# Optimization experiments

Measured on AMD Instinct MI355X. Metric: run time of the kernel, lower is better.

## Reference

```python
import jax, jax.numpy as jnp
import numpy as np

B, L, D, H, DFF, V, NL = 8, 512, 1024, 16, 4096, 32000, 6
DH = D // H
EPS = 1e-5


def _layer_norm(x):
    # fresh nn.LayerNorm(d_model) each call: gamma=1, beta=0
    mu = jnp.mean(x, axis=-1, keepdims=True)
    var = jnp.var(x, axis=-1, keepdims=True)
    return (x - mu) / jnp.sqrt(var + EPS)


def _positional_encoding(seq_len, d_model, dtype):
    position = jnp.arange(seq_len, dtype=jnp.float32)[:, None]
    div_term = 1.0 / jnp.power(10000.0, jnp.arange(0, d_model, 2, dtype=jnp.float32) / d_model)
    pe = jnp.zeros((seq_len, d_model), dtype=jnp.float32)
    pe = pe.at[:, 0::2].set(jnp.sin(position * div_term))
    pe = pe.at[:, 1::2].set(jnp.cos(position * div_term))
    return pe.astype(dtype)  # [L, D]


def setup_inputs() -> dict:
    key = jax.random.key(0)
    ks = jax.random.split(key, 16)
    s = 0.02
    inp = {
        "sequence": jax.random.randint(ks[0], (B, L), 0, V),
        "segment_label": jax.random.randint(ks[1], (B, L), 0, 3),
        "tok_emb": jax.random.normal(ks[2], (V, D), jnp.float32) * s,
        "seg_emb": jax.random.normal(ks[3], (3, D), jnp.float32) * s,
        "Wq": jax.random.normal(ks[4], (NL, D, D), jnp.float32) * s,
        "bq": jnp.zeros((NL, D), jnp.float32),
        "Wk": jax.random.normal(ks[5], (NL, D, D), jnp.float32) * s,
        "bk": jnp.zeros((NL, D), jnp.float32),
        "Wv": jax.random.normal(ks[6], (NL, D, D), jnp.float32) * s,
        "bv": jnp.zeros((NL, D), jnp.float32),
        "Wo": jax.random.normal(ks[7], (NL, D, D), jnp.float32) * s,
        "bo": jnp.zeros((NL, D), jnp.float32),
        "W1": jax.random.normal(ks[8], (NL, D, DFF), jnp.float32) * s,
        "b1": jnp.zeros((NL, DFF), jnp.float32),
        "W2": jax.random.normal(ks[9], (NL, DFF, D), jnp.float32) * s,
        "b2": jnp.zeros((NL, D), jnp.float32),
    }
    return inp


def reference(sequence, segment_label, tok_emb, seg_emb, Wq, bq, Wk, bk, Wv, bv, Wo, bo, W1, b1, W2, b2):
    n_layers = Wq.shape[0]
    batch, seq_len = sequence.shape
    d_model = tok_emb.shape[1]
    n_heads = H
    dh = d_model // n_heads

    # pad mask: True where key token == 0; broadcast over heads and query positions
    pad = (sequence == 0)  # [B, Lk]
    mask = pad[:, None, None, :]  # [B, 1, 1, Lk]

    pe = _positional_encoding(seq_len, d_model, tok_emb.dtype)
    x = tok_emb[sequence] + pe[None, :, :] + seg_emb[segment_label]  # [B, L, D]

    for i in range(n_layers):
        residual = x
        # NOTE: original code uses a raw reshape [B, L, H*dh] -> [B, H, L, dh]
        # (no transpose); we replicate that exact math.
        q = (x @ Wq[i] + bq[i]).reshape(batch, n_heads, seq_len, dh)
        k = (x @ Wk[i] + bk[i]).reshape(batch, n_heads, seq_len, dh)
        v = (x @ Wv[i] + bv[i]).reshape(batch, n_heads, seq_len, dh)
        scores = jnp.einsum("bhqd,bhkd->bhqk", q, k) / jnp.sqrt(jnp.asarray(dh, x.dtype))
        scores = jnp.where(mask, jnp.asarray(-1e9, x.dtype), scores)
        attn = jax.nn.softmax(scores, axis=-1)
        context = jnp.einsum("bhqk,bhkd->bhqd", attn, v).reshape(batch, seq_len, n_heads * dh)
        out = context @ Wo[i] + bo[i]
        x = _layer_norm(out + residual)

        residual = x
        h = jax.nn.gelu(x @ W1[i] + b1[i], approximate=False)
        out = h @ W2[i] + b2[i]
        x = _layer_norm(residual + out)

    return x
```

## Files before the change

### kernel.cpp

```cpp
#include <hip/hip_runtime.h>
#include <cstdint>
#include <cstddef>

typedef unsigned short u16;
typedef __attribute__((ext_vector_type(8))) short short8;
typedef __attribute__((ext_vector_type(4))) float f32x4;

#define DEV __device__ __forceinline__

DEV float bf2f(u16 u) {
    union { float f; uint32_t i; } c; c.i = ((uint32_t)u) << 16; return c.f;
}
DEV u16 f2bf(float f) {
    union { float f; uint32_t i; } c; c.f = f;
    uint32_t r = c.i + 0x7FFF + ((c.i >> 16) & 1);
    return (u16)(r >> 16);
}

DEV void gload16(const void* g, void* l) {
    __builtin_amdgcn_global_load_lds(
        (const __attribute__((address_space(1))) void*)g,
        (__attribute__((address_space(3))) void*)l, 16, 0, 0);
}

template<int N> DEV void waitv() {
    if constexpr (N == 0)      asm volatile("s_waitcnt vmcnt(0)" ::: "memory");
    else if constexpr (N == 4) asm volatile("s_waitcnt vmcnt(4)" ::: "memory");
    else if constexpr (N == 8) asm volatile("s_waitcnt vmcnt(8)" ::: "memory");
    else                       asm volatile("s_waitcnt vmcnt(0)" ::: "memory");
}

template<int EPI>
__global__ __launch_bounds__(512)
void gemm_k64(const u16* __restrict__ Ablk, const u16* __restrict__ Bblk,
              void* __restrict__ C, const float* __restrict__ bias,
              const float* __restrict__ resid, int K, int Mtot, int Ntot)
{
    constexpr int THREADS = 512;
    constexpr int BM = 128, BN = 128;
    constexpr int MR = 4, NR = 2;
    __shared__ __align__(16) u16 As[3 * BM * 64];
    __shared__ __align__(16) u16 Bs[3 * BN * 64];

    const int tid = threadIdx.x, lane = tid & 63, wid = tid >> 6;
    const int wr = wid >> 2, wc = wid & 3;
    const int lr = lane & 15, lk = lane >> 4;
    const int m0 = blockIdx.x * BM, n0 = blockIdx.y * BN;
    const long planeA = (long)Mtot * 64, planeB = (long)Ntot * 64;

    f32x4 acc[MR][NR] = {};

    auto stageA = [&](int buf, int k0) {
#pragma unroll
        for (int i = 0; i < 2; ++i) {
            int ch = i * THREADS + tid;
            int row = ch >> 3, s = ch & 7, d = s ^ (row & 7);
            const u16* g = Ablk + (long)(k0 >> 6) * planeA + (long)(m0 + row) * 64 + d * 8;
            gload16(g, (char*)As + (size_t)buf * (BM * 128) + ch * 16);
        }
    };
    auto stageB = [&](int buf, int k0) {
#pragma unroll
        for (int i = 0; i < 2; ++i) {
            int ch = i * THREADS + tid;
            int row = ch >> 3, s = ch & 7, d = s ^ (row & 7);
            const u16* g = Bblk + (long)(k0 >> 6) * planeB + (long)(n0 + row) * 64 + d * 8;
            gload16(g, (char*)Bs + (size_t)buf * (BN * 128) + ch * 16);
        }
    };
    auto lds_off = [&](int row, int ks) -> int {
        return row * 64 + ((ks ^ (row & 7)) << 3);
    };

    const int nt = K >> 6;

    stageA(0, 0); stageB(0, 0);
    if (nt > 1) { stageA(1, 64); stageB(1, 64); }
    if (nt > 2) { stageA(2, 128); stageB(2, 128); }
    if (nt > 2)      waitv<8>();
    else if (nt > 1) waitv<4>();
    else             waitv<0>();
    __builtin_amdgcn_s_barrier();

    for (int k = 0; k < nt; ++k) {
        const int cur = k % 3;
        const u16* Ac = As + (size_t)cur * (BM * 64);
        const u16* Bc = Bs + (size_t)cur * (BN * 64);
        short8 af[2][MR], bf[2][NR];
#pragma unroll
        for (int h = 0; h < 2; ++h) {
#pragma unroll
            for (int m = 0; m < MR; ++m)
                af[h][m] = *(const short8*)(Ac + lds_off(wr * 64 + m * 16 + lr, h * 4 + lk));
#pragma unroll
            for (int n = 0; n < NR; ++n)
                bf[h][n] = *(const short8*)(Bc + lds_off(wc * 32 + n * 16 + lr, h * 4 + lk));
        }

        asm volatile("s_waitcnt lgkmcnt(0)" ::: "memory");
        __builtin_amdgcn_s_barrier();

        if (k + 3 < nt) { stageA(cur, (k + 3) * 64); stageB(cur, (k + 3) * 64); }

        __builtin_amdgcn_s_setprio(1);
#pragma unroll
        for (int h = 0; h < 2; ++h)
#pragma unroll
            for (int m = 0; m < MR; ++m)
#pragma unroll
                for (int n = 0; n < NR; ++n)
                    acc[m][n] = __builtin_amdgcn_mfma_f32_16x16x32_bf16(af[h][m], bf[h][n], acc[m][n], 0, 0, 0);
        __builtin_amdgcn_s_setprio(0);

        if (k + 1 < nt) {
            if (k + 4 <= nt)      waitv<8>();
            else if (k + 3 == nt) waitv<4>();
            else                  waitv<0>();
            __builtin_amdgcn_s_barrier();
        }
    }

#pragma unroll
    for (int m = 0; m < MR; ++m) {
        const int rowb = m0 + wr * 64 + m * 16 + (lane >> 4) * 4;
#pragma unroll
        for (int n = 0; n < NR; ++n) {
            const int col = n0 + wc * 32 + n * 16 + lr;
            const float bv = bias[col];
#pragma unroll
            for (int j = 0; j < 4; ++j) {
                float v = acc[m][n][j];
                if (EPI == 1) {
                    const long idx = (long)(rowb + j) * 1024 + col;
                    ((float*)C)[idx] = v + bv + resid[idx];
                } else if (EPI == 5) {
                    const long qidx = (long)(col >> 10) * 4194304L
                                    + (long)(rowb + j) * 1024 + (col & 1023);
                    ((u16*)C)[qidx] = f2bf(v + bv);
                } else {
                    float t = v + bv;
                    ((u16*)C)[(long)(col >> 6) * 262144L + (long)(rowb + j) * 64 + (col & 63)]
                        = f2bf(0.5f * t * (1.0f + erff(t * 0.70710678118654752f)));
                }
            }
        }
    }
}

__global__ __launch_bounds__(512)
void attn_kernel(const u16* __restrict__ Qb, const u16* __restrict__ Kb,
                 const u16* __restrict__ vt, const int* __restrict__ seq,
                 u16* __restrict__ ctxB)
{
    __shared__ __align__(16) u16 Ss[64 * 512];
    const int tid = threadIdx.x, lane = tid & 63, wid = tid >> 6;
    const int bh = blockIdx.y;
    const int b  = bh >> 4;
    const int q0 = blockIdx.x << 6;
    const u16* Qh = Qb + ((long)bh << 15) + (long)q0 * 64;
    const u16* Kh = Kb + ((long)bh << 15);
    const u16* Vh = vt + ((long)bh << 15);
    const int lr = lane & 15, lk = lane >> 4;

    f32x4 sacc[4][4] = {};
    {
        short8 af[4], bf[4];
#pragma unroll
        for (int s = 0; s < 2; ++s) {
#pragma unroll
            for (int m = 0; m < 4; ++m)
                af[m] = *(const short8*)(Qh + (long)(m * 16 + lr) * 64 + s * 32 + lk * 8);
#pragma unroll
            for (int n = 0; n < 4; ++n)
                bf[n] = *(const short8*)(Kh + (long)(wid * 64 + n * 16 + lr) * 64 + s * 32 + lk * 8);
#pragma unroll
            for (int m = 0; m < 4; ++m)
#pragma unroll
                for (int n = 0; n < 4; ++n)
                    sacc[m][n] = __builtin_amdgcn_mfma_f32_16x16x32_bf16(af[m], bf[n], sacc[m][n], 0, 0, 0);
        }
    }
#pragma unroll
    for (int m = 0; m < 4; ++m) {
#pragma unroll
        for (int n = 0; n < 4; ++n) {
            const int k = wid * 64 + n * 16 + lr;
#pragma unroll
            for (int j = 0; j < 4; ++j) {
                const int q = m * 16 + (lane >> 4) * 4 + j;
                const int col = (((k >> 3) ^ (q & 7)) << 3) | (k & 7);
                Ss[q * 512 + col] = f2bf(sacc[m][n][j] * 0.125f);
            }
        }
    }
    __syncthreads();

    const int* sq = seq + (b << 9) + (lane << 3);
    int msk[8];
#pragma unroll
    for (int i = 0; i < 8; ++i) msk[i] = sq[i];
#pragma unroll
    for (int r = 0; r < 8; ++r) {
        const int q = wid * 8 + r;
        u16* p = Ss + q * 512 + ((lane ^ (q & 7)) << 3);
        short8 raw = *(short8*)p;
        float v[8];
#pragma unroll
        for (int i = 0; i < 8; ++i)
            v[i] = (msk[i] == 0) ? -1e9f : bf2f((u16)raw[i]);
        float mx = v[0];
#pragma unroll
        for (int i = 1; i < 8; ++i) mx = fmaxf(mx, v[i]);
#pragma unroll
        for (int o = 32; o; o >>= 1) mx = fmaxf(mx, __shfl_xor(mx, o));
        float e[8], sum = 0.f;
#pragma unroll
        for (int i = 0; i < 8; ++i) { e[i] = expf(v[i] - mx); sum += e[i]; }
#pragma unroll
        for (int o = 32; o; o >>= 1) sum += __shfl_xor(sum, o);
        float rr = 1.0f / sum;
        short8 o8;
#pragma unroll
        for (int i = 0; i < 8; ++i) o8[i] = (short)f2bf(e[i] * rr);
        *(short8*)p = o8;
    }
    __syncthreads();

    const int wr = wid >> 1, wc2 = wid & 1;
    f32x4 pacc[2] = {};
#pragma unroll
    for (int ks = 0; ks < 16; ++ks) {
        const int qrow = wr * 16 + lr;
        short8 pa = *(const short8*)(Ss + qrow * 512 + (((ks * 4 + lk) ^ (qrow & 7)) << 3));
        short8 vb[2];
#pragma unroll
        for (int n = 0; n < 2; ++n) {
            const int d = wc2 * 32 + n * 16 + lr;
            vb[n] = *(const short8*)(Vh + (long)d * 512 + ks * 32 + lk * 8);
        }
#pragma unroll
        for (int n = 0; n < 2; ++n)
            pacc[n] = __builtin_amdgcn_mfma_f32_16x16x32_bf16(pa, vb[n], pacc[n], 0, 0, 0);
    }
#pragma unroll
    for (int n = 0; n < 2; ++n) {
        const int d = wc2 * 32 + n * 16 + lr;
#pragma unroll
        for (int j = 0; j < 4; ++j) {
            const int q = wr * 16 + (lane >> 4) * 4 + j;
            const long F = ((long)bh << 15) + (long)(q0 + q) * 64 + d;
            const long r = F >> 10;
            const int  c = (int)(F & 1023);
            ctxB[(long)(c >> 6) * 262144L + r * 64 + (c & 63)] = f2bf(pacc[n][j]);
        }
    }
}

__global__ __launch_bounds__(256)
void wconv_blk(const float* __restrict__ src, u16* __restrict__ dst,
               int N, int planeN, int row_off, long src_z, long dst_z)
{
    __shared__ __align__(16) float t[64][65];
    const int z = blockIdx.z;
    const int k0 = blockIdx.x * 64, n0 = blockIdx.y * 64;
    const float* s = src + (long)z * src_z + (long)k0 * N + n0;
    const int tid = threadIdx.x;
#pragma unroll
    for (int i = 0; i < 4; ++i) {
        int ch = (i << 8) + tid;
        int r = ch >> 4, c4 = ch & 15;
        float4 v = *(const float4*)(s + (long)r * N + c4 * 4);
        t[r][c4 * 4 + 0] = v.x; t[r][c4 * 4 + 1] = v.y;
        t[r][c4 * 4 + 2] = v.z; t[r][c4 * 4 + 3] = v.w;
    }
    __syncthreads();
    u16* d = dst + (long)z * dst_z + (long)blockIdx.x * planeN * 64 + (long)(row_off + n0) * 64;
#pragma unroll
    for (int i = 0; i < 4; ++i) {
        int ch = (i << 8) + tid;
        int c = ch >> 4, k4 = ch & 15;
        ushort4 o;
        o.x = f2bf(t[k4 * 4 + 0][c]);
        o.y = f2bf(t[k4 * 4 + 1][c]);
        o.z = f2bf(t[k4 * 4 + 2][c]);
        o.w = f2bf(t[k4 * 4 + 3][c]);
        *(ushort4*)(d + (long)c * 64 + k4 * 4) = o;
    }
}

__global__ __launch_bounds__(256)
void bconcat_kernel(const float* __restrict__ bq, const float* __restrict__ bk,
                    const float* __restrict__ bv, float* __restrict__ out)
{
    int i = blockIdx.x * 256 + threadIdx.x;
    int l = i / 3072, n = i % 3072;
    float v = (n < 1024) ? bq[l * 1024 + n]
            : (n < 2048) ? bk[l * 1024 + n - 1024]
                         : bv[l * 1024 + n - 2048];
    out[i] = v;
}

__global__ __launch_bounds__(256)
void embed_kernel(const int* __restrict__ seq, const int* __restrict__ seg,
                  const float* __restrict__ tok, const float* __restrict__ sege,
                  float* __restrict__ x, u16* __restrict__ xbB)
{
    long i = ((long)blockIdx.x << 8) + threadIdx.x;
    int d2 = (int)(i & 511);
    long bl = i >> 9;
    int l = (int)(bl & 511);
    int t = seq[bl];
    int g = seg[bl];
    float div = powf(10000.f, -(float)(2 * d2) * (1.0f / 1024.f));
    float arg = (float)l * div;
    float sv = sinf(arg), cv = cosf(arg);
    long toff = (long)t * 1024 + 2 * d2;
    long goff = (long)g * 1024 + 2 * d2;
    float x0 = tok[toff]     + sv + sege[goff];
    float x1 = tok[toff + 1] + cv + sege[goff + 1];
    long xo = (bl << 10) + 2 * d2;
    x[xo] = x0; x[xo + 1] = x1;
    const int c = 2 * d2;
    u16* p = xbB + (long)(c >> 6) * 262144L + bl * 64 + (c & 63);
    p[0] = f2bf(x0); p[1] = f2bf(x1);
}

__global__ __launch_bounds__(256)
void vtrans_kernel(const u16* __restrict__ Vb, u16* __restrict__ vt)
{
    __shared__ __align__(16) u16 t[64][72];
    const int bh = blockIdx.y;
    const int l0 = blockIdx.x << 6;
    const u16* src = Vb + ((long)bh << 15) + (long)l0 * 64;
    const int tid = threadIdx.x;
#pragma unroll
    for (int i = 0; i < 2; ++i) {
        int ch = (i << 8) + tid;
        int r = ch >> 3, c8 = ch & 7;
        short8 v = *(const short8*)(src + (long)r * 64 + (c8 << 3));
#pragma unroll
        for (int j = 0; j < 8; ++j) t[r][(c8 << 3) + j] = (u16)v[j];
    }
    __syncthreads();
    u16* d = vt + ((long)bh << 15) + l0;
#pragma unroll
    for (int i = 0; i < 2; ++i) {
        int ch = (i << 8) + tid;
        int dd = ch >> 3, l8 = ch & 7;
        short8 o;
#pragma unroll
        for (int j = 0; j < 8; ++j) o[j] = (short)t[(l8 << 3) + j][dd];
        *(short8*)(d + (long)dd * 512 + (l8 << 3)) = o;
    }
}

__global__ __launch_bounds__(256)
void ln_kernel(const float* __restrict__ in, float* __restrict__ xout, u16* __restrict__ xbB)
{
    const int row = blockIdx.x;
    const int tid = threadIdx.x;
    const float4 v = ((const float4*)(in + (long)row * 1024))[tid];
    float s = v.x + v.y + v.z + v.w;
#pragma unroll
    for (int o = 32; o; o >>= 1) s += __shfl_down(s, o);
    __shared__ float red[8];
    const int wid = tid >> 6, lane = tid & 63;
    if (lane == 0) red[wid] = s;
    __syncthreads();
    const float mean = (red[0] + red[1] + red[2] + red[3]) * (1.0f / 1024.f);
    const float dx = v.x - mean, dy = v.y - mean, dz = v.z - mean, dw = v.w - mean;
    float q = dx * dx + dy * dy + dz * dz + dw * dw;
#pragma unroll
    for (int o = 32; o; o >>= 1) q += __shfl_down(q, o);
    if (lane == 0) red[4 + wid] = q;
    __syncthreads();
    const float var = (red[4] + red[5] + red[6] + red[7]) * (1.0f / 1024.f);
    const float inv = rsqrtf(var + 1e-5f);
    float4 o4;
    o4.x = dx * inv; o4.y = dy * inv; o4.z = dz * inv; o4.w = dw * inv;
    ((float4*)(xout + (long)row * 1024))[tid] = o4;
    ushort4 ob;
    ob.x = f2bf(o4.x); ob.y = f2bf(o4.y); ob.z = f2bf(o4.z); ob.w = f2bf(o4.w);
    *(ushort4*)(xbB + (long)(tid >> 4) * 262144L + (long)row * 64 + (tid & 15) * 4) = ob;
}

extern "C" void kernel_launch(void* const* d_in, const int* in_sizes, int n_in,
                              void* d_out, int out_size, void* d_ws, size_t ws_size,
                              hipStream_t stream)
{
    const int*   seqp = (const int*)d_in[0];
    const int*   segp = (const int*)d_in[1];
    const float* tok  = (const float*)d_in[2];
    const float* sege = (const float*)d_in[3];
    const float* Wq = (const float*)d_in[4];  const float* bq = (const float*)d_in[5];
    const float* Wk = (const float*)d_in[6];  const float* bk = (const float*)d_in[7];
    const float* Wv = (const float*)d_in[8];  const float* bv = (const float*)d_in[9];
    const float* Wo = (const float*)d_in[10]; const float* bo = (const float*)d_in[11];
    const float* W1 = (const float*)d_in[12]; const float* b1 = (const float*)d_in[13];
    const float* W2 = (const float*)d_in[14]; const float* b2 = (const float*)d_in[15];

    char* w = (char*)d_ws;
    auto take = [&](size_t bytes) -> void* {
        void* p = (void*)w; w += (bytes + 255) & ~(size_t)255; return p;
    };
    float* x    = (float*)take(4096UL * 1024 * 4);
    u16*   xbB  = (u16*)  take(4096UL * 1024 * 2);
    float* tmp  = (float*)take(4096UL * 1024 * 4);
    u16*   hbuf = (u16*)  take(4096UL * 4096 * 2);
    u16*   qkv3 = (u16*)  take(3UL * 4096 * 1024 * 2);
    u16*   ctxB = (u16*)  take(4096UL * 1024 * 2);
    u16*   vt   = (u16*)  take(128UL * 64 * 512 * 2);
    u16*   qkvwB= (u16*)  take(6UL * 3072 * 1024 * 2);
    u16*   woB  = (u16*)  take(6UL * 1024 * 1024 * 2);
    u16*   w1B  = (u16*)  take(6UL * 4096 * 1024 * 2);
    u16*   w2B  = (u16*)  take(6UL * 1024 * 4096 * 2);
    float* bqkv = (float*)take(6UL * 3072 * 4);

    u16* Qb = qkv3;
    u16* Kb = qkv3 + 4194304L;
    u16* Vb = qkv3 + 8388608L;

    bconcat_kernel<<<72, 256, 0, stream>>>(bq, bk, bv, bqkv);
    wconv_blk<<<dim3(16, 16, 6), 256, 0, stream>>>(Wq, qkvwB, 1024, 3072, 0,    1048576L, 3145728L);
    wconv_blk<<<dim3(16, 16, 6), 256, 0, stream>>>(Wk, qkvwB, 1024, 3072, 1024, 1048576L, 3145728L);
    wconv_blk<<<dim3(16, 16, 6), 256, 0, stream>>>(Wv, qkvwB, 1024, 3072, 2048, 1048576L, 3145728L);
    wconv_blk<<<dim3(16, 16, 6), 256, 0, stream>>>(Wo, woB,   1024, 1024, 0,    1048576L, 1048576L);
    wconv_blk<<<dim3(16, 64, 6), 256, 0, stream>>>(W1, w1B,   4096, 4096, 0,    4194304L, 4194304L);
    wconv_blk<<<dim3(64, 16, 6), 256, 0, stream>>>(W2, w2B,   1024, 1024, 0,    4194304L, 4194304L);

    embed_kernel<<<8192, 256, 0, stream>>>(seqp, segp, tok, sege, x, xbB);

    for (int l = 0; l < 6; ++l) {
        gemm_k64<5><<<dim3(32, 24), 512, 0, stream>>>(
            xbB, qkvwB + (long)l * 3145728L, qkv3, bqkv + l * 3072, nullptr,
            1024, 4096, 3072);

        vtrans_kernel<<<dim3(8, 128), 256, 0, stream>>>(Vb, vt);

        attn_kernel<<<dim3(8, 128), 512, 0, stream>>>(Qb, Kb, vt, seqp, ctxB);

        gemm_k64<1><<<dim3(32, 8), 512, 0, stream>>>(
            ctxB, woB + (long)l * 1048576L, tmp, bo + l * 1024, x,
            1024, 4096, 1024);

        ln_kernel<<<4096, 256, 0, stream>>>(tmp, x, xbB);

        gemm_k64<6><<<dim3(32, 32), 512, 0, stream>>>(
            xbB, w1B + (long)l * 4194304L, hbuf, b1 + l * 4096, nullptr,
            1024, 4096, 4096);

        gemm_k64<1><<<dim3(32, 8), 512, 0, stream>>>(
            hbuf, w2B + (long)l * 4194304L, tmp, b2 + l * 1024, x,
            4096, 4096, 1024);

        ln_kernel<<<4096, 256, 0, stream>>>(tmp, (l == 5) ? (float*)d_out : x, xbB);
    }
}
```

Before: 1.899 ms.

## Add 256x256-tile GEMM kernel for QKV and FFN1 projections

Adds a new GEMM kernel with 256x256 output tiles, a K-step of 32 and a three-stage LDS buffer. It is used for the QKV projection and the first FFN GEMM. Each wave holds an 8x4 grid of MFMA accumulators, and global loads are split and interleaved between the two halves of the MFMA work. The goal is more operand reuse per LDS byte and less global traffic per output. The cost is fewer blocks: 192 for QKV, which does not fill every CU in one wave, and higher register pressure. The old kernel is reduced to the residual-add epilogue only.

```diff
diff --git a/kernel.cpp b/kernel.cpp
--- a/kernel.cpp
+++ b/kernel.cpp
@@ -32,8 +32,126 @@
 
 template<int EPI>
 __global__ __launch_bounds__(512)
+void gemm256_blk(const u16* __restrict__ Ablk, const u16* __restrict__ Bblk,
+                 void* __restrict__ C, const float* __restrict__ bias,
+                 int K, int Mtot, int Ntot)
+{
+    constexpr int THREADS = 512;
+    constexpr int BM = 256, BN = 256, BK = 32;
+    constexpr int MR = 8, NR = 4;
+    __shared__ __align__(16) u16 As[3 * BM * BK];
+    __shared__ __align__(16) u16 Bs[3 * BN * BK];
+
+    const int tid = threadIdx.x, lane = tid & 63, wid = tid >> 6;
+    const int wr = wid >> 2, wc = wid & 3;
+    const int lr = lane & 15, lk = lane >> 4;
+    const int m0 = blockIdx.x * BM, n0 = blockIdx.y * BN;
+    const long planeA = (long)Mtot * 64, planeB = (long)Ntot * 64;
+
+    f32x4 acc[MR][NR] = {};
+
+    auto stageA = [&](int buf, int k0) {
+        const long base = (long)(k0 >> 6) * planeA + (k0 & 32);
+#pragma unroll
+        for (int i = 0; i < 2; ++i) {
+            int ch = i * THREADS + tid;
+            int rp = ch >> 3, s = ch & 7, d = s ^ (rp & 7);
+            const u16* g = Ablk + base + (long)(m0 + ((rp << 1) | (d & 1))) * 64 + ((d >> 1) << 3);
+            gload16(g, (char*)As + (size_t)buf * (BM * BK * 2) + ch * 16);
+        }
+    };
+    auto stageB = [&](int buf, int k0) {
+        const long base = (long)(k0 >> 6) * planeB + (k0 & 32);
+#pragma unroll
+        for (int i = 0; i < 2; ++i) {
+            int ch = i * THREADS + tid;
+            int rp = ch >> 3, s = ch & 7, d = s ^ (rp & 7);
+            const u16* g = Bblk + base + (long)(n0 + ((rp << 1) | (d & 1))) * 64 + ((d >> 1) << 3);
+            gload16(g, (char*)Bs + (size_t)buf * (BN * BK * 2) + ch * 16);
+        }
+    };
+    auto lds_off = [&](int row) -> int {
+        int rp = row >> 1;
+        int s  = ((lk << 1) | (row & 1)) ^ (rp & 7);
+        return rp * 64 + s * 8;
+    };
+
+    const int nt = K >> 5;
+
+    stageA(0, 0); stageB(0, 0);
+    if (nt > 1) { stageA(1, BK); stageB(1, BK); }
+    if (nt > 1) waitv<4>(); else waitv<0>();
+    __builtin_amdgcn_s_barrier();
+
+    for (int k = 0; k < nt; ++k) {
+        const int cur = k % 3;
+        const int nxt = (k + 2) % 3;
+        const u16* Ac = As + (size_t)cur * (BM * BK);
+        const u16* Bc = Bs + (size_t)cur * (BN * BK);
+        short8 af[MR], bf[NR];
+
+#pragma unroll
+        for (int n = 0; n < NR; ++n)
+            bf[n] = *(const short8*)(Bc + lds_off(wc * 64 + n * 16 + lr));
+#pragma unroll
+        for (int m = 0; m < 4; ++m)
+            af[m] = *(const short8*)(Ac + lds_off(wr * 128 + m * 16 + lr));
+        if (k + 2 < nt) stageA(nxt, (k + 2) * BK);
+        asm volatile("s_waitcnt lgkmcnt(0)" ::: "memory");
+        __builtin_amdgcn_s_setprio(1);
+#pragma unroll
+        for (int m = 0; m < 4; ++m)
+#pragma unroll
+            for (int n = 0; n < NR; ++n)
+                acc[m][n] = __builtin_amdgcn_mfma_f32_16x16x32_bf16(af[m], bf[n], acc[m][n], 0, 0, 0);
+        __builtin_amdgcn_s_setprio(0);
+
+#pragma unroll
+        for (int m = 4; m < 8; ++m)
+            af[m] = *(const short8*)(Ac + lds_off(wr * 128 + m * 16 + lr));
+        if (k + 2 < nt) stageB(nxt, (k + 2) * BK);
+        asm volatile("s_waitcnt lgkmcnt(0)" ::: "memory");
+        __builtin_amdgcn_s_setprio(1);
+#pragma unroll
+        for (int m = 4; m < 8; ++m)
+#pragma unroll
+            for (int n = 0; n < NR; ++n)
+                acc[m][n] = __builtin_amdgcn_mfma_f32_16x16x32_bf16(af[m], bf[n], acc[m][n], 0, 0, 0);
+        __builtin_amdgcn_s_setprio(0);
+
+        if (k + 1 < nt) {
+            if (k + 2 < nt) waitv<4>(); else waitv<0>();
+            __builtin_amdgcn_s_barrier();
+        }
+    }
+
+#pragma unroll
+    for (int m = 0; m < MR; ++m) {
+        const int rowb = m0 + wr * 128 + m * 16 + (lane >> 4) * 4;
+#pragma unroll
+        for (int n = 0; n < NR; ++n) {
+            const int col = n0 + wc * 64 + n * 16 + lr;
+            const float bv = bias[col];
+#pragma unroll
+            for (int j = 0; j < 4; ++j) {
+                float v = acc[m][n][j];
+                if (EPI == 6) {
+                    float t = v + bv;
+                    ((u16*)C)[(long)(col >> 6) * 262144L + (long)(rowb + j) * 64 + (col & 63)]
+                        = f2bf(0.5f * t * (1.0f + erff(t * 0.70710678118654752f)));
+                } else {
+                    const long qidx = (long)(col >> 10) * 4194304L
+                                    + (long)(rowb + j) * 1024 + (col & 1023);
+                    ((u16*)C)[qidx] = f2bf(v + bv);
+                }
+            }
+        }
+    }
+}
+
+__global__ __launch_bounds__(512)
 void gemm_k64(const u16* __restrict__ Ablk, const u16* __restrict__ Bblk,
-              void* __restrict__ C, const float* __restrict__ bias,
+              float* __restrict__ C, const float* __restrict__ bias,
               const float* __restrict__ resid, int K, int Mtot, int Ntot)
 {
     constexpr int THREADS = 512;
@@ -129,19 +247,8 @@
             const float bv = bias[col];
 #pragma unroll
             for (int j = 0; j < 4; ++j) {
-                float v = acc[m][n][j];
-                if (EPI == 1) {
-                    const long idx = (long)(rowb + j) * 1024 + col;
-                    ((float*)C)[idx] = v + bv + resid[idx];
-                } else if (EPI == 5) {
-                    const long qidx = (long)(col >> 10) * 4194304L
-                                    + (long)(rowb + j) * 1024 + (col & 1023);
-                    ((u16*)C)[qidx] = f2bf(v + bv);
-                } else {
-                    float t = v + bv;
-                    ((u16*)C)[(long)(col >> 6) * 262144L + (long)(rowb + j) * 64 + (col & 63)]
-                        = f2bf(0.5f * t * (1.0f + erff(t * 0.70710678118654752f)));
-                }
+                const long idx = (long)(rowb + j) * 1024 + col;
+                C[idx] = acc[m][n][j] + bv + resid[idx];
             }
         }
     }
@@ -431,25 +538,25 @@
     embed_kernel<<<8192, 256, 0, stream>>>(seqp, segp, tok, sege, x, xbB);
 
     for (int l = 0; l < 6; ++l) {
-        gemm_k64<5><<<dim3(32, 24), 512, 0, stream>>>(
-            xbB, qkvwB + (long)l * 3145728L, qkv3, bqkv + l * 3072, nullptr,
+        gemm256_blk<5><<<dim3(16, 12), 512, 0, stream>>>(
+            xbB, qkvwB + (long)l * 3145728L, qkv3, bqkv + l * 3072,
             1024, 4096, 3072);
 
         vtrans_kernel<<<dim3(8, 128), 256, 0, stream>>>(Vb, vt);
 
         attn_kernel<<<dim3(8, 128), 512, 0, stream>>>(Qb, Kb, vt, seqp, ctxB);
 
-        gemm_k64<1><<<dim3(32, 8), 512, 0, stream>>>(
+        gemm_k64<<<dim3(32, 8), 512, 0, stream>>>(
             ctxB, woB + (long)l * 1048576L, tmp, bo + l * 1024, x,
             1024, 4096, 1024);
 
         ln_kernel<<<4096, 256, 0, stream>>>(tmp, x, xbB);
 
-        gemm_k64<6><<<dim3(32, 32), 512, 0, stream>>>(
-            xbB, w1B + (long)l * 4194304L, hbuf, b1 + l * 4096, nullptr,
+        gemm256_blk<6><<<dim3(16, 16), 512, 0, stream>>>(
+            xbB, w1B + (long)l * 4194304L, hbuf, b1 + l * 4096,
             1024, 4096, 4096);
 
-        gemm_k64<1><<<dim3(32, 8), 512, 0, stream>>>(
+        gemm_k64<<<dim3(32, 8), 512, 0, stream>>>(
             hbuf, w2B + (long)l * 4194304L, tmp, b2 + l * 1024, x,
             4096, 4096, 1024);
 
```

Result: faster. 1.634 ms (-14.0%).
